# Kernel optimization log

Hardware: AMD Instinct MI355X
Metric: run time of the kernel (lower is better)

The kernel has to match this reference:

```python
import jax, jax.numpy as jnp
import numpy as np

B, T, D, U, W = 8, 1024, 1024, 1024, 2  # batch, seq_len, input_dim, units, window_size


def setup_inputs() -> dict:
    key = jax.random.key(0)
    k1, k2 = jax.random.split(key)
    x = jax.random.normal(k1, (B, T, D), dtype=jnp.float32)
    # keras 'uniform' initializer: U(-0.05, 0.05); kernel squeezed from (W,1,D,3U) to (W,D,3U)
    kernel = jax.random.uniform(k2, (W, D, 3 * U), dtype=jnp.float32, minval=-0.05, maxval=0.05)
    bias = jnp.zeros((3 * U,), dtype=jnp.float32)  # 'zero' initializer
    return {"x": x, "kernel": kernel, "bias": bias}


def reference(x, kernel, bias):
    Wk, Din, U3 = kernel.shape
    Un = U3 // 3
    Tn = x.shape[1]
    # causal temporal padding (window_size-1 on the left), then valid windowed conv
    xp = jnp.pad(x, ((0, 0), (Wk - 1, 0), (0, 0)))
    # gates[b,t] = sum_k xp[b,t+k] @ kernel[k] + bias  -> [B,T,3U]
    gates = sum(jnp.einsum('btd,du->btu', xp[:, k:k + Tn], kernel[k]) for k in range(Wk)) + bias
    z = jnp.tanh(gates[..., :Un])
    f = jax.nn.sigmoid(gates[..., Un:2 * Un])
    o = jax.nn.sigmoid(gates[..., 2 * Un:])

    def step(h, zfo):
        zt, ft, ot = zfo
        h_new = ot * (ft * h + (1.0 - ft) * zt)
        return h_new, h_new

    h0 = jnp.zeros((x.shape[0], Un), dtype=x.dtype)
    _, hs = jax.lax.scan(step, h0, (z.swapaxes(0, 1), f.swapaxes(0, 1), o.swapaxes(0, 1)))
    return hs.swapaxes(0, 1)  # [B,T,U] (return_sequences=True)
```

## Files before the change

kernel.cpp:

```cpp
#include <hip/hip_runtime.h>
#include <hip/hip_bf16.h>

typedef __bf16 bf16x8 __attribute__((ext_vector_type(8)));
typedef float f32x4 __attribute__((ext_vector_type(4)));

#define GLOBAL_AS(p) ((const __attribute__((address_space(1))) void*)(p))
#define LDS_AS(p)    ((__attribute__((address_space(3))) void*)(p))

static __device__ __forceinline__ unsigned short f2bf(float f) {
    union { float f; unsigned u; } v; v.f = f;
    unsigned r = v.u + 0x7FFFu + ((v.u >> 16) & 1u);
    return (unsigned short)(r >> 16);
}

__global__ void zero_page(float4* __restrict__ z) {
    z[threadIdx.x * 4 + 0] = make_float4(0.f, 0.f, 0.f, 0.f);
    z[threadIdx.x * 4 + 1] = make_float4(0.f, 0.f, 0.f, 0.f);
    z[threadIdx.x * 4 + 2] = make_float4(0.f, 0.f, 0.f, 0.f);
    z[threadIdx.x * 4 + 3] = make_float4(0.f, 0.f, 0.f, 0.f);
}

__global__ void prep_xb(const float* __restrict__ x, unsigned short* __restrict__ xb) {
    const int m = blockIdx.x;
    const int c = threadIdx.x * 4;
    float4 v = *reinterpret_cast<const float4*>(x + (size_t)m * 1024 + c);
    ushort4 b = make_ushort4(f2bf(v.x), f2bf(v.y), f2bf(v.z), f2bf(v.w));
    *reinterpret_cast<ushort4*>(xb + (size_t)m * 1024 + c) = b;
}

__global__ void prep_kt(const float* __restrict__ K, unsigned short* __restrict__ KT) {
    __shared__ float tile[64][65];
    const int bi = blockIdx.x;
    const int bj = blockIdx.y;
    const int tx = threadIdx.x & 63;
    const int ty = threadIdx.x >> 6;

#pragma unroll
    for (int i = 0; i < 16; ++i) {
        int r = ty * 16 + i;
        tile[r][tx] = K[(size_t)(bi * 64 + r) * 3072 + bj * 64 + tx];
    }
    __syncthreads();
#pragma unroll
    for (int i = 0; i < 16; ++i) {
        int r = ty * 16 + i;
        KT[(size_t)(bj * 64 + r) * 2048 + bi * 64 + tx] = f2bf(tile[tx][r]);
    }
}

__global__ __launch_bounds__(256, 2)
void gemm_gates(const unsigned short* __restrict__ xb,
                const unsigned short* __restrict__ BT,
                const unsigned short* __restrict__ zpage,
                const float* __restrict__ bias,
                float* __restrict__ G) {
    __shared__ __align__(16) unsigned short As[128 * 64];
    __shared__ __align__(16) unsigned short Bs[128 * 64];

    const int tid  = threadIdx.x;
    const int lane = tid & 63;
    const int wid  = tid >> 6;
    const int wr   = wid >> 1, wc = wid & 1;
    const int m0   = blockIdx.y * 128;
    const int n0   = blockIdx.x * 128;

    f32x4 acc[4][4] = {};

    const int sr = lane >> 3;
    const int sc = lane & 7;

    const unsigned short* srcA_lo[4];
    const unsigned short* srcA_hi[4];
    const unsigned short* srcB[4];
#pragma unroll
    for (int i = 0; i < 4; ++i) {
        const int r  = wid * 32 + i * 8 + sr;
        const int cc = sc ^ (r & 7);
        const int srow = m0 + r;
        srcA_hi[i] = xb + (size_t)srow * 1024 + cc * 8;
        srcA_lo[i] = ((srow & 1023) == 0) ? (zpage + cc * 8)
                                          : (xb + (size_t)(srow - 1) * 1024 + cc * 8);
        srcB[i]    = BT + (size_t)(n0 + r) * 2048 + cc * 8;
    }

    for (int kt = 0; kt < 32; ++kt) {
        const int kb = kt * 64;
#pragma unroll
        for (int i = 0; i < 4; ++i) {
            const int r0 = wid * 32 + i * 8;
            const unsigned short* sa = (kt < 16) ? (srcA_lo[i] + kb)
                                                 : (srcA_hi[i] + (kb - 1024));
            __builtin_amdgcn_global_load_lds(GLOBAL_AS(sa),          LDS_AS(As + r0 * 64), 16, 0, 0);
            __builtin_amdgcn_global_load_lds(GLOBAL_AS(srcB[i] + kb), LDS_AS(Bs + r0 * 64), 16, 0, 0);
        }
        __syncthreads();

#pragma unroll
        for (int ks = 0; ks < 2; ++ks) {
            bf16x8 af[4], bg[4];
#pragma unroll
            for (int m = 0; m < 4; ++m) {
                const int row = wr * 64 + m * 16 + (lane & 15);
                const int c   = ks * 4 + (lane >> 4);
                const int p   = c ^ (row & 7);
                af[m] = *reinterpret_cast<const bf16x8*>(As + row * 64 + p * 8);
            }
#pragma unroll
            for (int n = 0; n < 4; ++n) {
                const int row = wc * 64 + n * 16 + (lane & 15);
                const int c   = ks * 4 + (lane >> 4);
                const int p   = c ^ (row & 7);
                bg[n] = *reinterpret_cast<const bf16x8*>(Bs + row * 64 + p * 8);
            }
#pragma unroll
            for (int m = 0; m < 4; ++m)
#pragma unroll
                for (int n = 0; n < 4; ++n)
                    acc[m][n] = __builtin_amdgcn_mfma_f32_16x16x32_bf16(af[m], bg[n], acc[m][n], 0, 0, 0);
        }
        __syncthreads();
    }

    const int rgn = n0 >> 10;
#pragma unroll
    for (int m = 0; m < 4; ++m) {
#pragma unroll
        for (int n = 0; n < 4; ++n) {
            const int col = n0 + wc * 64 + n * 16 + (lane & 15);
            const float bv = bias[col];
#pragma unroll
            for (int v = 0; v < 4; ++v) {
                const int row = m0 + wr * 64 + m * 16 + ((lane >> 4) * 4) + v;
                const float g = acc[m][n][v] + bv;
                float val;
                if (rgn == 0) {
                    float s = 1.0f / (1.0f + __expf(-2.0f * g));
                    val = 2.0f * s - 1.0f;
                } else {
                    val = 1.0f / (1.0f + __expf(-g));
                }
                G[(size_t)row * 3072 + col] = val;
            }
        }
    }
}

__global__ void scan_pass1(const float* __restrict__ G, float2* __restrict__ AB) {
    const int bid = blockIdx.x;
    const int ug  = bid & 3;
    const int c   = (bid >> 2) & 7;
    const int b   = bid >> 5;
    const int u   = ug * 256 + threadIdx.x;
    const float* g = G + (size_t)(b * 1024 + c * 128) * 3072 + u;
    float A = 1.f, Bv = 0.f;
#pragma unroll 8
    for (int i = 0; i < 128; ++i) {
        const float zv = g[(size_t)i * 3072];
        const float fv = g[(size_t)i * 3072 + 1024];
        const float ov = g[(size_t)i * 3072 + 2048];
        const float a  = ov * fv;
        const float bb = ov * (1.f - fv) * zv;
        A  = a * A;
        Bv = a * Bv + bb;
    }
    AB[(size_t)(b * 8 + c) * 1024 + u] = make_float2(A, Bv);
}

__global__ void scan_pass23(const float* __restrict__ G, const float2* __restrict__ AB,
                            float* __restrict__ out) {
    const int b  = blockIdx.x >> 3;
    const int ug = blockIdx.x & 7;
    const int c  = threadIdx.x >> 7;
    const int ui = threadIdx.x & 127;
    const int u  = ug * 128 + ui;

    float h = 0.f;
    for (int j = 0; j < c; ++j) {
        float2 p = AB[(size_t)(b * 8 + j) * 1024 + u];
        h = p.x * h + p.y;
    }
    const float* g = G + (size_t)(b * 1024 + c * 128) * 3072 + u;
    float* o = out + (size_t)(b * 1024 + c * 128) * 1024 + u;
#pragma unroll 8
    for (int i = 0; i < 128; ++i) {
        const float zv = g[(size_t)i * 3072];
        const float fv = g[(size_t)i * 3072 + 1024];
        const float ov = g[(size_t)i * 3072 + 2048];
        h = ov * (fv * h + (1.f - fv) * zv);
        o[(size_t)i * 1024] = h;
    }
}

extern "C" void kernel_launch(void* const* d_in, const int* in_sizes, int n_in,
                              void* d_out, int out_size, void* d_ws, size_t ws_size,
                              hipStream_t stream) {
    const float* x    = (const float*)d_in[0];
    const float* kern = (const float*)d_in[1];
    const float* bias = (const float*)d_in[2];
    float* out = (float*)d_out;

    char* ws = (char*)d_ws;
    unsigned short* xb   = (unsigned short*)ws;
    unsigned short* KT   = (unsigned short*)(ws + 16777216);
    float* G             = (float*)(ws + 29360128);
    float2* AB           = (float2*)(ws + 130023424);
    unsigned short* zpg  = (unsigned short*)(ws + 130547712);

    zero_page<<<1, 64, 0, stream>>>((float4*)zpg);
    prep_xb<<<dim3(8192), dim3(256), 0, stream>>>(x, xb);
    prep_kt<<<dim3(32, 48), dim3(256), 0, stream>>>(kern, KT);
    gemm_gates<<<dim3(24, 64), dim3(256), 0, stream>>>(xb, KT, zpg, bias, G);
    scan_pass1<<<dim3(256), dim3(256), 0, stream>>>(G, AB);
    scan_pass23<<<dim3(64), dim3(1024), 0, stream>>>(G, AB, out);
}
```

Baseline: 177.6 us.

## Store gate activations in fp16 and use zero-padded bf16 input layout

The gate activations buffer G is now written as fp16 instead of fp32, halving the traffic between the GEMM epilogue and both scan passes. The bf16 copy of x gets a zero row in front of each batch, which makes the causal shift a plain pointer offset and removes both the zero_page kernel and the per-tile branch in the A loads. This costs some gate precision, since fp16 holds values in [-1,1] with about 11 bits of mantissa, and the error can build up through the recurrence.

```diff
diff --git a/kernel.cpp b/kernel.cpp
--- a/kernel.cpp
+++ b/kernel.cpp
@@ -13,19 +13,18 @@
     return (unsigned short)(r >> 16);
 }
 
-__global__ void zero_page(float4* __restrict__ z) {
-    z[threadIdx.x * 4 + 0] = make_float4(0.f, 0.f, 0.f, 0.f);
-    z[threadIdx.x * 4 + 1] = make_float4(0.f, 0.f, 0.f, 0.f);
-    z[threadIdx.x * 4 + 2] = make_float4(0.f, 0.f, 0.f, 0.f);
-    z[threadIdx.x * 4 + 3] = make_float4(0.f, 0.f, 0.f, 0.f);
-}
-
-__global__ void prep_xb(const float* __restrict__ x, unsigned short* __restrict__ xb) {
-    const int m = blockIdx.x;
+__global__ void prep_xb(const float* __restrict__ x, unsigned short* __restrict__ xb2) {
+    const int bid = blockIdx.x;
     const int c = threadIdx.x * 4;
-    float4 v = *reinterpret_cast<const float4*>(x + (size_t)m * 1024 + c);
-    ushort4 b = make_ushort4(f2bf(v.x), f2bf(v.y), f2bf(v.z), f2bf(v.w));
-    *reinterpret_cast<ushort4*>(xb + (size_t)m * 1024 + c) = b;
+    if (bid < 8192) {
+        const int dst = bid + (bid >> 10) + 1;
+        float4 v = *reinterpret_cast<const float4*>(x + (size_t)bid * 1024 + c);
+        ushort4 b = make_ushort4(f2bf(v.x), f2bf(v.y), f2bf(v.z), f2bf(v.w));
+        *reinterpret_cast<ushort4*>(xb2 + (size_t)dst * 1024 + c) = b;
+    } else {
+        const int zr = (bid - 8192) * 1025;
+        *reinterpret_cast<ushort4*>(xb2 + (size_t)zr * 1024 + c) = make_ushort4(0, 0, 0, 0);
+    }
 }
 
 __global__ void prep_kt(const float* __restrict__ K, unsigned short* __restrict__ KT) {
@@ -49,11 +48,10 @@
 }
 
 __global__ __launch_bounds__(256, 2)
-void gemm_gates(const unsigned short* __restrict__ xb,
+void gemm_gates(const unsigned short* __restrict__ xb2,
                 const unsigned short* __restrict__ BT,
-                const unsigned short* __restrict__ zpage,
                 const float* __restrict__ bias,
-                float* __restrict__ G) {
+                _Float16* __restrict__ G) {
     __shared__ __align__(16) unsigned short As[128 * 64];
     __shared__ __align__(16) unsigned short Bs[128 * 64];
 
@@ -69,18 +67,15 @@
     const int sr = lane >> 3;
     const int sc = lane & 7;
 
-    const unsigned short* srcA_lo[4];
-    const unsigned short* srcA_hi[4];
+    const unsigned short* srcA[4];
     const unsigned short* srcB[4];
 #pragma unroll
     for (int i = 0; i < 4; ++i) {
         const int r  = wid * 32 + i * 8 + sr;
         const int cc = sc ^ (r & 7);
-        const int srow = m0 + r;
-        srcA_hi[i] = xb + (size_t)srow * 1024 + cc * 8;
-        srcA_lo[i] = ((srow & 1023) == 0) ? (zpage + cc * 8)
-                                          : (xb + (size_t)(srow - 1) * 1024 + cc * 8);
-        srcB[i]    = BT + (size_t)(n0 + r) * 2048 + cc * 8;
+        const int m  = m0 + r;
+        srcA[i] = xb2 + (size_t)(m + (m >> 10)) * 1024 + cc * 8;
+        srcB[i] = BT  + (size_t)(n0 + r) * 2048 + cc * 8;
     }
 
     for (int kt = 0; kt < 32; ++kt) {
@@ -88,9 +83,7 @@
 #pragma unroll
         for (int i = 0; i < 4; ++i) {
             const int r0 = wid * 32 + i * 8;
-            const unsigned short* sa = (kt < 16) ? (srcA_lo[i] + kb)
-                                                 : (srcA_hi[i] + (kb - 1024));
-            __builtin_amdgcn_global_load_lds(GLOBAL_AS(sa),          LDS_AS(As + r0 * 64), 16, 0, 0);
+            __builtin_amdgcn_global_load_lds(GLOBAL_AS(srcA[i] + kb), LDS_AS(As + r0 * 64), 16, 0, 0);
             __builtin_amdgcn_global_load_lds(GLOBAL_AS(srcB[i] + kb), LDS_AS(Bs + r0 * 64), 16, 0, 0);
         }
         __syncthreads();
@@ -139,25 +132,25 @@
                 } else {
                     val = 1.0f / (1.0f + __expf(-g));
                 }
-                G[(size_t)row * 3072 + col] = val;
+                G[(size_t)row * 3072 + col] = (_Float16)val;
             }
         }
     }
 }
 
-__global__ void scan_pass1(const float* __restrict__ G, float2* __restrict__ AB) {
+__global__ void scan_pass1(const _Float16* __restrict__ G, float2* __restrict__ AB) {
     const int bid = blockIdx.x;
     const int ug  = bid & 3;
     const int c   = (bid >> 2) & 7;
     const int b   = bid >> 5;
     const int u   = ug * 256 + threadIdx.x;
-    const float* g = G + (size_t)(b * 1024 + c * 128) * 3072 + u;
+    const _Float16* g = G + (size_t)(b * 1024 + c * 128) * 3072 + u;
     float A = 1.f, Bv = 0.f;
 #pragma unroll 8
     for (int i = 0; i < 128; ++i) {
-        const float zv = g[(size_t)i * 3072];
-        const float fv = g[(size_t)i * 3072 + 1024];
-        const float ov = g[(size_t)i * 3072 + 2048];
+        const float zv = (float)g[(size_t)i * 3072];
+        const float fv = (float)g[(size_t)i * 3072 + 1024];
+        const float ov = (float)g[(size_t)i * 3072 + 2048];
         const float a  = ov * fv;
         const float bb = ov * (1.f - fv) * zv;
         A  = a * A;
@@ -166,7 +159,7 @@
     AB[(size_t)(b * 8 + c) * 1024 + u] = make_float2(A, Bv);
 }
 
-__global__ void scan_pass23(const float* __restrict__ G, const float2* __restrict__ AB,
+__global__ void scan_pass23(const _Float16* __restrict__ G, const float2* __restrict__ AB,
                             float* __restrict__ out) {
     const int b  = blockIdx.x >> 3;
     const int ug = blockIdx.x & 7;
@@ -179,13 +172,13 @@
         float2 p = AB[(size_t)(b * 8 + j) * 1024 + u];
         h = p.x * h + p.y;
     }
-    const float* g = G + (size_t)(b * 1024 + c * 128) * 3072 + u;
+    const _Float16* g = G + (size_t)(b * 1024 + c * 128) * 3072 + u;
     float* o = out + (size_t)(b * 1024 + c * 128) * 1024 + u;
 #pragma unroll 8
     for (int i = 0; i < 128; ++i) {
-        const float zv = g[(size_t)i * 3072];
-        const float fv = g[(size_t)i * 3072 + 1024];
-        const float ov = g[(size_t)i * 3072 + 2048];
+        const float zv = (float)g[(size_t)i * 3072];
+        const float fv = (float)g[(size_t)i * 3072 + 1024];
+        const float ov = (float)g[(size_t)i * 3072 + 2048];
         h = ov * (fv * h + (1.f - fv) * zv);
         o[(size_t)i * 1024] = h;
     }
@@ -200,16 +193,14 @@
     float* out = (float*)d_out;
 
     char* ws = (char*)d_ws;
-    unsigned short* xb   = (unsigned short*)ws;
-    unsigned short* KT   = (unsigned short*)(ws + 16777216);
-    float* G             = (float*)(ws + 29360128);
-    float2* AB           = (float2*)(ws + 130023424);
-    unsigned short* zpg  = (unsigned short*)(ws + 130547712);
-
-    zero_page<<<1, 64, 0, stream>>>((float4*)zpg);
-    prep_xb<<<dim3(8192), dim3(256), 0, stream>>>(x, xb);
+    unsigned short* xb2 = (unsigned short*)ws;
+    unsigned short* KT  = (unsigned short*)(ws + 16793600);
+    _Float16* G         = (_Float16*)(ws + 29376512);
+    float2* AB          = (float2*)(ws + 79708160);
+
+    prep_xb<<<dim3(8200), dim3(256), 0, stream>>>(x, xb2);
     prep_kt<<<dim3(32, 48), dim3(256), 0, stream>>>(kern, KT);
-    gemm_gates<<<dim3(24, 64), dim3(256), 0, stream>>>(xb, KT, zpg, bias, G);
+    gemm_gates<<<dim3(24, 64), dim3(256), 0, stream>>>(xb2, KT, bias, G);
     scan_pass1<<<dim3(256), dim3(256), 0, stream>>>(G, AB);
     scan_pass23<<<dim3(64), dim3(1024), 0, stream>>>(G, AB, out);
 }
```

Measured after the change: 158.6 us. 10.7% less time.
